# Kernel optimization log

Measured on AMD Instinct MI355X. Metric: run time of the kernel, lower is better.

## Reference

```python
import jax, jax.numpy as jnp
import numpy as np

# Config (matches init_kwargs)
LOW_T = 100      # low_res_timesteps
HIGH_T = 2000    # high_res_timesteps
FEAT = 6         # feature_dim
HID = 256        # student_hidden_dim
NUM_CLASSES = 10
LBL_DIM = 16
UP = HIGH_T // LOW_T  # upsampling_factor = 20
B = 4096


def setup_inputs() -> dict:
    key = jax.random.key(0)
    ks = jax.random.split(key, 20)

    def lin(k, fan_in, fan_out):
        # torch nn.Linear default init: U(-1/sqrt(fan_in), 1/sqrt(fan_in))
        kw, kb = jax.random.split(k)
        bound = 1.0 / np.sqrt(fan_in)
        W = jax.random.uniform(kw, (fan_in, fan_out), jnp.float32, -bound, bound)
        b = jax.random.uniform(kb, (fan_out,), jnp.float32, -bound, bound)
        return W, b

    W1, b1 = lin(ks[0], LOW_T * FEAT, HID * 2)
    W2, b2 = lin(ks[1], HID * 2, HID)
    W3, b3 = lin(ks[2], HID, HID // 2)
    dec_in = HID // 2 + LBL_DIM
    W4, b4 = lin(ks[3], dec_in, HID)
    W5, b5 = lin(ks[4], HID, HID * 2)
    W6, b6 = lin(ks[5], HID * 2, HIGH_T * FEAT)
    emb = jax.random.normal(ks[6], (NUM_CLASSES, LBL_DIM), jnp.float32)

    low_res_data = jax.random.normal(ks[7], (B, LOW_T, FEAT), jnp.float32)
    labels = jax.random.randint(ks[8], (B,), 0, NUM_CLASSES, jnp.int64)
    return {
        'low_res_data': low_res_data, 'labels': labels,
        'W1': W1, 'b1': b1, 'W2': W2, 'b2': b2, 'W3': W3, 'b3': b3,
        'W4': W4, 'b4': b4, 'W5': W5, 'b5': b5, 'W6': W6, 'b6': b6,
        'emb': emb,
    }


def reference(low_res_data, labels, W1, b1, W2, b2, W3, b3, W4, b4, W5, b5, W6, b6, emb):
    batch = low_res_data.shape[0]
    # Encoder MLP (dropout is identity in eval mode)
    x = low_res_data.reshape(batch, -1)                     # [B, LOW_T*FEAT]
    h = jax.nn.relu(x @ W1 + b1)
    h = jax.nn.relu(h @ W2 + b2)
    feat = h @ W3 + b3                                      # [B, HID//2]
    # Label conditioning
    feat = jnp.concatenate([feat, emb[labels]], axis=-1)    # [B, HID//2 + LBL_DIM]
    # Decoder MLP
    h = jax.nn.relu(feat @ W4 + b4)
    h = jax.nn.relu(h @ W5 + b5)
    decoded = (h @ W6 + b6).reshape(batch, HIGH_T, FEAT)    # [B, H, F]

    # Vectorized constraint enforcement + smoothing (replaces per-timestep python loop):
    #  - at anchor timesteps t = i*UP: output = low_res_data[:, i]
    #  - between anchors i and i+1: lin = (1-a)*low[i] + a*low[i+1];
    #      out = lin + 0.2 * (decoded - lin)
    #  - after the last anchor interval ((LOW_T-1)*UP < t < HIGH_T): out = decoded
    t = jnp.arange(HIGH_T)
    seg = jnp.clip(t // UP, 0, LOW_T - 2)                   # segment index per timestep
    alpha = ((t - seg * UP) / UP).astype(decoded.dtype)     # [H], 0 at anchors, 1 at seg end
    start = low_res_data[:, seg]                            # [B, H, F]
    end = low_res_data[:, seg + 1]                          # [B, H, F]
    a = alpha[None, :, None]
    lin_interp = (1.0 - a) * start + a * end                # equals low point at anchors
    blend = lin_interp + 0.2 * (decoded - lin_interp)
    is_anchor = (t % UP == 0)[None, :, None]
    in_interior = (t < (LOW_T - 1) * UP)[None, :, None]
    enhanced = jnp.where(is_anchor, lin_interp, jnp.where(in_interior, blend, decoded))
    return enhanced
```

## Files before the change

### kernel.cpp

```cpp
#include <hip/hip_runtime.h>
#include <hip/hip_bf16.h>

typedef __attribute__((ext_vector_type(8))) short bf16x8;
typedef __attribute__((ext_vector_type(4))) float f32x4;
typedef __attribute__((ext_vector_type(8))) unsigned short u16x8;
typedef unsigned short ushort_t;
typedef unsigned int u32;

__device__ __forceinline__ ushort_t f2b(float f) {
    u32 u = __builtin_bit_cast(u32, f);
    u += 0x7FFFu + ((u >> 16) & 1u);
    return (ushort_t)(u >> 16);
}

__device__ __forceinline__ void gload_lds16(const void* g, void* l) {
    __builtin_amdgcn_global_load_lds(
        (const __attribute__((address_space(1))) u32*)g,
        (__attribute__((address_space(3))) u32*)l, 16, 0, 0);
}

struct TrDesc { const float* src; ushort_t* dst; int K, N, Kpad, Npad, base, nx; };
struct TrArgs { TrDesc d[6]; const float* low; ushort_t* xb; int trbase; };

__global__ __launch_bounds__(256) void prep_kernel(TrArgs a) {
    const int bid = blockIdx.x, tid = threadIdx.x;
    if (bid >= a.trbase) {
        int idx = (bid - a.trbase) * 256 + tid;
        int b = idx / 76, c = idx - b * 76;
        ushort_t* dp = a.xb + (size_t)b * 608 + c * 8;
        u16x8 o;
        if (c < 75) {
            const float* sp = a.low + (size_t)b * 600 + c * 8;
            f32x4 v0 = *(const f32x4*)sp, v1 = *(const f32x4*)(sp + 4);
            #pragma unroll
            for (int j = 0; j < 4; ++j) { o[j] = f2b(v0[j]); o[4 + j] = f2b(v1[j]); }
        } else {
            #pragma unroll
            for (int j = 0; j < 8; ++j) o[j] = 0;
        }
        *(u16x8*)dp = o;
        return;
    }
    __shared__ float T[64][65];
    int w = 0;
    #pragma unroll
    for (int i = 1; i < 6; ++i) if (bid >= a.d[i].base) w = i;
    const TrDesc d = a.d[w];
    const int local = bid - d.base;
    const int n0 = (local % d.nx) * 64, k0 = (local / d.nx) * 64;
    #pragma unroll
    for (int it = 0; it < 16; ++it) {
        int idx = it * 256 + tid;
        int r = idx >> 6, c = idx & 63;
        int k = k0 + r, n = n0 + c;
        T[c][r] = (k < d.K && n < d.N) ? d.src[(size_t)k * d.N + n] : 0.f;
    }
    __syncthreads();
    #pragma unroll
    for (int it = 0; it < 16; ++it) {
        int idx = it * 256 + tid;
        int r = idx >> 6, c = idx & 63;
        int n = n0 + r, k = k0 + c;
        if (k < d.Kpad)
            d.dst[(size_t)n * d.Kpad + k] = f2b(T[r][c]);
    }
}

template<int EPI>
__global__ __launch_bounds__(256, 4) void gemm64(
    const ushort_t* __restrict__ A, const ushort_t* __restrict__ Bt,
    const float* __restrict__ bias, ushort_t* __restrict__ Cb,
    const int* __restrict__ lbl, const float* __restrict__ emb,
    int K, int Nreal, int ldc)
{
    __shared__ ushort_t As[2][64 * 32];
    __shared__ ushort_t Bs[2][64 * 32];
    const int tid = threadIdx.x;
    const int wave = tid >> 6, lane = tid & 63;
    const int l15 = lane & 15, g = lane >> 4;
    const int wr = wave >> 1, wc = wave & 1;
    const int m0 = blockIdx.y * 64, n0 = blockIdx.x * 64;

    f32x4 acc[2][2] = {};

    const int p0 = tid * 16;
    const int row0 = p0 >> 6;
    const int k0s = (((p0 & 63) ^ (((row0 >> 1) & 3) << 4)) >> 1);
    const ushort_t* a0 = A + (size_t)(m0 + row0) * K + k0s;
    const ushort_t* b0 = Bt + (size_t)(n0 + row0) * K + k0s;

    char* AsB = (char*)As + wave * 1024;
    char* BsB = (char*)Bs + wave * 1024;

    const int sxor = ((l15 >> 1) & 3) << 4;
    const ushort_t* ardA = &As[0][0] + (((wr * 32 + l15) * 64 + ((g * 16) ^ sxor)) >> 1);
    const ushort_t* brdB = &Bs[0][0] + (((wc * 32 + l15) * 64 + ((g * 16) ^ sxor)) >> 1);

    const int nk = K >> 5;
    gload_lds16(a0, AsB); gload_lds16(b0, BsB);
    a0 += 32; b0 += 32;
    __syncthreads();
    #pragma unroll 2
    for (int kk = 0; kk < nk; ++kk) {
        const int cur = kk & 1, nxt = cur ^ 1;
        if (kk + 1 < nk) {
            gload_lds16(a0, AsB + nxt * 4096);
            gload_lds16(b0, BsB + nxt * 4096);
            a0 += 32; b0 += 32;
        }
        bf16x8 af[2], bf[2];
        #pragma unroll
        for (int i = 0; i < 2; ++i) af[i] = *(const bf16x8*)(ardA + cur * 2048 + i * 512);
        #pragma unroll
        for (int j = 0; j < 2; ++j) bf[j] = *(const bf16x8*)(brdB + cur * 2048 + j * 512);
        #pragma unroll
        for (int i = 0; i < 2; ++i)
            #pragma unroll
            for (int j = 0; j < 2; ++j)
                acc[i][j] = __builtin_amdgcn_mfma_f32_16x16x32_bf16(af[i], bf[j], acc[i][j], 0, 0, 0);
        __syncthreads();
    }

    #pragma unroll
    for (int i = 0; i < 2; ++i)
        #pragma unroll
        for (int r = 0; r < 4; ++r) {
            int row = m0 + wr * 32 + i * 16 + g * 4 + r;
            #pragma unroll
            for (int j = 0; j < 2; ++j) {
                int col = n0 + wc * 32 + j * 16 + l15;
                if (col >= Nreal) continue;
                float v = acc[i][j][r] + bias[col];
                if (EPI == 0) v = fmaxf(v, 0.f);
                Cb[(size_t)row * ldc + col] = f2b(v);
            }
        }

    if (EPI == 1 && blockIdx.x == 0) {
        #pragma unroll
        for (int q = 0; q < 8; ++q) {
            int e = tid + q * 256;
            int row = m0 + (e >> 5), c = e & 31;
            float v = c < 16 ? emb[(size_t)lbl[row] * 16 + c] : 0.f;
            Cb[(size_t)row * ldc + 128 + c] = f2b(v);
        }
    }
}

__global__ __launch_bounds__(256, 4) void gemm128_l6(
    const ushort_t* __restrict__ A, const ushort_t* __restrict__ Bt,
    const float* __restrict__ bias, float* __restrict__ Cf,
    const float* __restrict__ low, int K)
{
    __shared__ ushort_t As[2][128 * 32];
    __shared__ ushort_t Bs[2][128 * 32];
    const int tid = threadIdx.x;
    const int wave = tid >> 6, lane = tid & 63;
    const int l15 = lane & 15, g = lane >> 4;
    const int wr = wave >> 1, wc = wave & 1;
    const int m0 = blockIdx.y * 128, n0 = blockIdx.x * 128;

    f32x4 acc[4][4] = {};

    const int p0 = tid * 16;
    const int row0 = p0 >> 6;
    const int k0s = (((p0 & 63) ^ (((row0 >> 1) & 3) << 4)) >> 1);
    const int p1 = 4096 + tid * 16;
    const int row1 = p1 >> 6;
    const int k1s = (((p1 & 63) ^ (((row1 >> 1) & 3) << 4)) >> 1);

    const ushort_t* a0 = A + (size_t)(m0 + row0) * K + k0s;
    const ushort_t* a1 = A + (size_t)(m0 + row1) * K + k1s;
    const ushort_t* b0 = Bt + (size_t)(n0 + row0) * K + k0s;
    const ushort_t* b1 = Bt + (size_t)(n0 + row1) * K + k1s;

    char* AsB = (char*)As + wave * 1024;
    char* BsB = (char*)Bs + wave * 1024;

    const int sxor = ((l15 >> 1) & 3) << 4;
    const ushort_t* ardA = &As[0][0] + (((wr * 64 + l15) * 64 + ((g * 16) ^ sxor)) >> 1);
    const ushort_t* brdB = &Bs[0][0] + (((wc * 64 + l15) * 64 + ((g * 16) ^ sxor)) >> 1);

    const int nk = K >> 5;
    gload_lds16(a0, AsB); gload_lds16(a1, AsB + 4096);
    gload_lds16(b0, BsB); gload_lds16(b1, BsB + 4096);
    a0 += 32; a1 += 32; b0 += 32; b1 += 32;
    __syncthreads();
    #pragma unroll 2
    for (int kk = 0; kk < nk; ++kk) {
        const int cur = kk & 1, nxt = cur ^ 1;
        if (kk + 1 < nk) {
            gload_lds16(a0, AsB + nxt * 8192);
            gload_lds16(a1, AsB + nxt * 8192 + 4096);
            gload_lds16(b0, BsB + nxt * 8192);
            gload_lds16(b1, BsB + nxt * 8192 + 4096);
            a0 += 32; a1 += 32; b0 += 32; b1 += 32;
        }
        bf16x8 af[4], bf[4];
        #pragma unroll
        for (int i = 0; i < 4; ++i) af[i] = *(const bf16x8*)(ardA + cur * 4096 + i * 512);
        #pragma unroll
        for (int j = 0; j < 4; ++j) bf[j] = *(const bf16x8*)(brdB + cur * 4096 + j * 512);
        #pragma unroll
        for (int i = 0; i < 4; ++i)
            #pragma unroll
            for (int j = 0; j < 4; ++j)
                acc[i][j] = __builtin_amdgcn_mfma_f32_16x16x32_bf16(af[i], bf[j], acc[i][j], 0, 0, 0);
        __syncthreads();
    }

    float bvv[4]; int offv[4]; float alphav[4];
    bool anch[4], interi[4], valid[4];
    #pragma unroll
    for (int j = 0; j < 4; ++j) {
        int col = n0 + wc * 64 + j * 16 + l15;
        valid[j] = col < 12000;
        int cc = valid[j] ? col : 0;
        bvv[j] = bias[cc];
        int t = cc / 6, f = cc - t * 6;
        int seg = t / 20; if (seg > 98) seg = 98;
        offv[j] = seg * 6 + f;
        alphav[j] = (float)(t - seg * 20) * 0.05f;
        anch[j] = (t % 20) == 0;
        interi[j] = t < 1980;
    }
    const int colb = n0 + wc * 64 + l15;
    #pragma unroll
    for (int i = 0; i < 4; ++i)
        #pragma unroll
        for (int r = 0; r < 4; ++r) {
            const int row = m0 + wr * 64 + i * 16 + g * 4 + r;
            const float* lrow = low + (size_t)row * 600;
            float* orow = Cf + (size_t)row * 12000;
            #pragma unroll
            for (int j = 0; j < 4; ++j) {
                if (!valid[j]) continue;
                float s = lrow[offv[j]], e = lrow[offv[j] + 6];
                float lin = (1.f - alphav[j]) * s + alphav[j] * e;
                float dec = acc[i][j][r] + bvv[j];
                float res = anch[j] ? lin : (interi[j] ? lin + 0.2f * (dec - lin) : dec);
                __builtin_nontemporal_store(res, &orow[colb + j * 16]);
            }
        }
}

extern "C" void kernel_launch(void* const* d_in, const int* in_sizes, int n_in,
                              void* d_out, int out_size, void* d_ws, size_t ws_size,
                              hipStream_t stream) {
    const float* low = (const float*)d_in[0];
    const int*   lbl = (const int*)d_in[1];
    const float* W1 = (const float*)d_in[2];  const float* b1 = (const float*)d_in[3];
    const float* W2 = (const float*)d_in[4];  const float* b2 = (const float*)d_in[5];
    const float* W3 = (const float*)d_in[6];  const float* b3 = (const float*)d_in[7];
    const float* W4 = (const float*)d_in[8];  const float* b4 = (const float*)d_in[9];
    const float* W5 = (const float*)d_in[10]; const float* b5 = (const float*)d_in[11];
    const float* W6 = (const float*)d_in[12]; const float* b6 = (const float*)d_in[13];
    const float* emb = (const float*)d_in[14];
    float* out = (float*)d_out;

    char* ws = (char*)d_ws;
    size_t off = 0;
    auto alloc = [&](size_t elems) {
        ushort_t* p = (ushort_t*)(ws + off);
        off = (off + elems * 2 + 255) & ~(size_t)255;
        return p;
    };
    ushort_t* xb  = alloc((size_t)4096 * 608);
    ushort_t* w1t = alloc((size_t)512 * 608);
    ushort_t* w2t = alloc((size_t)256 * 512);
    ushort_t* w3t = alloc((size_t)128 * 256);
    ushort_t* w4t = alloc((size_t)256 * 160);
    ushort_t* w5t = alloc((size_t)512 * 256);
    ushort_t* w6t = alloc((size_t)12032 * 512);
    ushort_t* h1  = alloc((size_t)4096 * 512);
    ushort_t* h2  = alloc((size_t)4096 * 256);
    ushort_t* fc  = alloc((size_t)4096 * 160);
    ushort_t* h4  = alloc((size_t)4096 * 256);
    ushort_t* h5  = alloc((size_t)4096 * 512);

    TrArgs ta;
    int base = 0;
    auto mk = [&](int i, const float* s, ushort_t* d, int K, int N, int Kp, int Np) {
        int nx = Np / 64, ny = (Kp + 63) / 64;
        ta.d[i] = TrDesc{s, d, K, N, Kp, Np, base, nx};
        base += nx * ny;
    };
    mk(0, W1, w1t, 600, 512, 608, 512);
    mk(1, W2, w2t, 512, 256, 512, 256);
    mk(2, W3, w3t, 256, 128, 256, 128);
    mk(3, W4, w4t, 144, 256, 160, 256);
    mk(4, W5, w5t, 256, 512, 256, 512);
    mk(5, W6, w6t, 512, 12000, 512, 12032);
    ta.low = low; ta.xb = xb; ta.trbase = base;
    const int castx_blocks = (4096 * 76) / 256;

    prep_kernel<<<dim3(base + castx_blocks), 256, 0, stream>>>(ta);

    gemm64<0><<<dim3(8, 64), 256, 0, stream>>>(xb, w1t, b1, h1, nullptr, nullptr, 608, 512, 512);
    gemm64<0><<<dim3(4, 64), 256, 0, stream>>>(h1, w2t, b2, h2, nullptr, nullptr, 512, 256, 256);
    gemm64<1><<<dim3(2, 64), 256, 0, stream>>>(h2, w3t, b3, fc, lbl, emb, 256, 128, 160);
    gemm64<0><<<dim3(4, 64), 256, 0, stream>>>(fc, w4t, b4, h4, nullptr, nullptr, 160, 256, 256);
    gemm64<0><<<dim3(8, 64), 256, 0, stream>>>(h4, w5t, b5, h5, nullptr, nullptr, 256, 512, 512);
    gemm128_l6<<<dim3(94, 32), 256, 0, stream>>>(h5, w6t, b6, out, low, 512);
}
```

Baseline: 392.0 us.

## Fuse prep and first five GEMMs into cooperative kernel; enlarge final GEMM tile

Replaces the prep kernel and five small GEMM launches with one cooperative persistent kernel that uses grid.sync between layers, cutting launch gaps and tail effects. The final layer GEMM moves from 128x128 tiles with 256 threads to 256x256 tiles with 512 threads, which raises data reuse per block but cuts the grid to 752 blocks and adds register pressure. Nontemporal output stores become plain stores. Grid syncs carry their own cost, and the cooperative launch with 512 blocks must fit co-resident on the device.

Result: slower. 983.8 us (+151.0%).

```diff
diff --git a/kernel.cpp b/kernel.cpp
--- a/kernel.cpp
+++ b/kernel.cpp
@@ -1,5 +1,8 @@
 #include <hip/hip_runtime.h>
 #include <hip/hip_bf16.h>
+#include <hip/hip_cooperative_groups.h>
+
+namespace cg = cooperative_groups;
 
 typedef __attribute__((ext_vector_type(8))) short bf16x8;
 typedef __attribute__((ext_vector_type(4))) float f32x4;
@@ -20,66 +23,27 @@
 }
 
 struct TrDesc { const float* src; ushort_t* dst; int K, N, Kpad, Npad, base, nx; };
-struct TrArgs { TrDesc d[6]; const float* low; ushort_t* xb; int trbase; };
-
-__global__ __launch_bounds__(256) void prep_kernel(TrArgs a) {
-    const int bid = blockIdx.x, tid = threadIdx.x;
-    if (bid >= a.trbase) {
-        int idx = (bid - a.trbase) * 256 + tid;
-        int b = idx / 76, c = idx - b * 76;
-        ushort_t* dp = a.xb + (size_t)b * 608 + c * 8;
-        u16x8 o;
-        if (c < 75) {
-            const float* sp = a.low + (size_t)b * 600 + c * 8;
-            f32x4 v0 = *(const f32x4*)sp, v1 = *(const f32x4*)(sp + 4);
-            #pragma unroll
-            for (int j = 0; j < 4; ++j) { o[j] = f2b(v0[j]); o[4 + j] = f2b(v1[j]); }
-        } else {
-            #pragma unroll
-            for (int j = 0; j < 8; ++j) o[j] = 0;
-        }
-        *(u16x8*)dp = o;
-        return;
-    }
-    __shared__ float T[64][65];
-    int w = 0;
-    #pragma unroll
-    for (int i = 1; i < 6; ++i) if (bid >= a.d[i].base) w = i;
-    const TrDesc d = a.d[w];
-    const int local = bid - d.base;
-    const int n0 = (local % d.nx) * 64, k0 = (local / d.nx) * 64;
-    #pragma unroll
-    for (int it = 0; it < 16; ++it) {
-        int idx = it * 256 + tid;
-        int r = idx >> 6, c = idx & 63;
-        int k = k0 + r, n = n0 + c;
-        T[c][r] = (k < d.K && n < d.N) ? d.src[(size_t)k * d.N + n] : 0.f;
-    }
-    __syncthreads();
-    #pragma unroll
-    for (int it = 0; it < 16; ++it) {
-        int idx = it * 256 + tid;
-        int r = idx >> 6, c = idx & 63;
-        int n = n0 + r, k = k0 + c;
-        if (k < d.Kpad)
-            d.dst[(size_t)n * d.Kpad + k] = f2b(T[r][c]);
-    }
-}
-
-template<int EPI>
-__global__ __launch_bounds__(256, 4) void gemm64(
+
+struct CoopArgs {
+    TrDesc d[6];
+    const float* low; const int* lbl; const float* emb;
+    const float *b1, *b2, *b3, *b4, *b5;
+    ushort_t *xb, *h1, *h2, *fc, *h4, *h5;
+    ushort_t *w1t, *w2t, *w3t, *w4t, *w5t;
+    int trbase, total0;
+};
+
+template<int RELU>
+__device__ __forceinline__ void tile_gemm64(
     const ushort_t* __restrict__ A, const ushort_t* __restrict__ Bt,
     const float* __restrict__ bias, ushort_t* __restrict__ Cb,
-    const int* __restrict__ lbl, const float* __restrict__ emb,
-    int K, int Nreal, int ldc)
+    int K, int Nreal, int ldc, int m0, int n0, char* smem, int tid)
 {
-    __shared__ ushort_t As[2][64 * 32];
-    __shared__ ushort_t Bs[2][64 * 32];
-    const int tid = threadIdx.x;
+    ushort_t* As = (ushort_t*)smem;
+    ushort_t* Bs = (ushort_t*)(smem + 8192);
     const int wave = tid >> 6, lane = tid & 63;
     const int l15 = lane & 15, g = lane >> 4;
     const int wr = wave >> 1, wc = wave & 1;
-    const int m0 = blockIdx.y * 64, n0 = blockIdx.x * 64;
 
     f32x4 acc[2][2] = {};
 
@@ -89,18 +53,17 @@
     const ushort_t* a0 = A + (size_t)(m0 + row0) * K + k0s;
     const ushort_t* b0 = Bt + (size_t)(n0 + row0) * K + k0s;
 
-    char* AsB = (char*)As + wave * 1024;
-    char* BsB = (char*)Bs + wave * 1024;
+    char* AsB = smem + wave * 1024;
+    char* BsB = smem + 8192 + wave * 1024;
 
     const int sxor = ((l15 >> 1) & 3) << 4;
-    const ushort_t* ardA = &As[0][0] + (((wr * 32 + l15) * 64 + ((g * 16) ^ sxor)) >> 1);
-    const ushort_t* brdB = &Bs[0][0] + (((wc * 32 + l15) * 64 + ((g * 16) ^ sxor)) >> 1);
+    const ushort_t* ardA = As + (((wr * 32 + l15) * 64 + ((g * 16) ^ sxor)) >> 1);
+    const ushort_t* brdB = Bs + (((wc * 32 + l15) * 64 + ((g * 16) ^ sxor)) >> 1);
 
     const int nk = K >> 5;
     gload_lds16(a0, AsB); gload_lds16(b0, BsB);
     a0 += 32; b0 += 32;
     __syncthreads();
-    #pragma unroll 2
     for (int kk = 0; kk < nk; ++kk) {
         const int cur = kk & 1, nxt = cur ^ 1;
         if (kk + 1 < nk) {
@@ -131,41 +94,115 @@
                 int col = n0 + wc * 32 + j * 16 + l15;
                 if (col >= Nreal) continue;
                 float v = acc[i][j][r] + bias[col];
-                if (EPI == 0) v = fmaxf(v, 0.f);
+                if (RELU) v = fmaxf(v, 0.f);
                 Cb[(size_t)row * ldc + col] = f2b(v);
             }
         }
-
-    if (EPI == 1 && blockIdx.x == 0) {
-        #pragma unroll
-        for (int q = 0; q < 8; ++q) {
-            int e = tid + q * 256;
-            int row = m0 + (e >> 5), c = e & 31;
-            float v = c < 16 ? emb[(size_t)lbl[row] * 16 + c] : 0.f;
-            Cb[(size_t)row * ldc + 128 + c] = f2b(v);
-        }
-    }
-}
-
-__global__ __launch_bounds__(256, 4) void gemm128_l6(
+}
+
+__global__ __launch_bounds__(256) void coop_chain(CoopArgs a) {
+    __shared__ __align__(16) char smem[16640];
+    const int tid = threadIdx.x;
+    const int bid = blockIdx.x;
+    const int nb = gridDim.x;
+    cg::grid_group grid = cg::this_grid();
+
+    for (int u = bid; u < a.total0; u += nb) {
+        if (u < a.trbase) {
+            float (*T)[65] = (float(*)[65])smem;
+            int w = 0;
+            #pragma unroll
+            for (int i = 1; i < 6; ++i) if (u >= a.d[i].base) w = i;
+            const TrDesc d = a.d[w];
+            const int local = u - d.base;
+            const int n0 = (local % d.nx) * 64, k0 = (local / d.nx) * 64;
+            #pragma unroll
+            for (int it = 0; it < 16; ++it) {
+                int idx = it * 256 + tid;
+                int r = idx >> 6, c = idx & 63;
+                int k = k0 + r, n = n0 + c;
+                T[c][r] = (k < d.K && n < d.N) ? d.src[(size_t)k * d.N + n] : 0.f;
+            }
+            __syncthreads();
+            #pragma unroll
+            for (int it = 0; it < 16; ++it) {
+                int idx = it * 256 + tid;
+                int r = idx >> 6, c = idx & 63;
+                int n = n0 + r, k = k0 + c;
+                if (k < d.Kpad)
+                    d.dst[(size_t)n * d.Kpad + k] = f2b(T[r][c]);
+            }
+            __syncthreads();
+        } else {
+            int idx = (u - a.trbase) * 256 + tid;
+            int b = idx / 76, c = idx - b * 76;
+            ushort_t* dp = a.xb + (size_t)b * 608 + c * 8;
+            u16x8 o;
+            if (c < 75) {
+                const float* sp = a.low + (size_t)b * 600 + c * 8;
+                f32x4 v0 = *(const f32x4*)sp, v1 = *(const f32x4*)(sp + 4);
+                #pragma unroll
+                for (int j = 0; j < 4; ++j) { o[j] = f2b(v0[j]); o[4 + j] = f2b(v1[j]); }
+            } else {
+                #pragma unroll
+                for (int j = 0; j < 8; ++j) o[j] = 0;
+            }
+            *(u16x8*)dp = o;
+            __syncthreads();
+        }
+    }
+    __threadfence();
+    grid.sync();
+
+    for (int t = bid; t < 512; t += nb)
+        tile_gemm64<1>(a.xb, a.w1t, a.b1, a.h1, 608, 512, 512, (t >> 3) * 64, (t & 7) * 64, smem, tid);
+    __threadfence();
+    grid.sync();
+
+    for (int t = bid; t < 256; t += nb)
+        tile_gemm64<1>(a.h1, a.w2t, a.b2, a.h2, 512, 256, 256, (t >> 2) * 64, (t & 3) * 64, smem, tid);
+    __threadfence();
+    grid.sync();
+
+    for (int t = bid; t < 128; t += nb)
+        tile_gemm64<0>(a.h2, a.w3t, a.b3, a.fc, 256, 128, 160, (t >> 1) * 64, (t & 1) * 64, smem, tid);
+    for (int u = bid; u < 512; u += nb) {
+        int e = u * 256 + tid;
+        int row = e >> 5, c = e & 31;
+        float v = c < 16 ? a.emb[(size_t)a.lbl[row] * 16 + c] : 0.f;
+        a.fc[(size_t)row * 160 + 128 + c] = f2b(v);
+    }
+    __threadfence();
+    grid.sync();
+
+    for (int t = bid; t < 256; t += nb)
+        tile_gemm64<1>(a.fc, a.w4t, a.b4, a.h4, 160, 256, 256, (t >> 2) * 64, (t & 3) * 64, smem, tid);
+    __threadfence();
+    grid.sync();
+
+    for (int t = bid; t < 512; t += nb)
+        tile_gemm64<1>(a.h4, a.w5t, a.b5, a.h5, 256, 512, 512, (t >> 3) * 64, (t & 7) * 64, smem, tid);
+}
+
+__global__ __launch_bounds__(512) void gemm256_l6(
     const ushort_t* __restrict__ A, const ushort_t* __restrict__ Bt,
     const float* __restrict__ bias, float* __restrict__ Cf,
     const float* __restrict__ low, int K)
 {
-    __shared__ ushort_t As[2][128 * 32];
-    __shared__ ushort_t Bs[2][128 * 32];
+    __shared__ ushort_t As[2][256 * 32];
+    __shared__ ushort_t Bs[2][256 * 32];
     const int tid = threadIdx.x;
     const int wave = tid >> 6, lane = tid & 63;
     const int l15 = lane & 15, g = lane >> 4;
-    const int wr = wave >> 1, wc = wave & 1;
-    const int m0 = blockIdx.y * 128, n0 = blockIdx.x * 128;
-
-    f32x4 acc[4][4] = {};
+    const int wr = wave >> 2, wc = wave & 3;
+    const int m0 = blockIdx.y * 256, n0 = blockIdx.x * 256;
+
+    f32x4 acc[8][4] = {};
 
     const int p0 = tid * 16;
     const int row0 = p0 >> 6;
     const int k0s = (((p0 & 63) ^ (((row0 >> 1) & 3) << 4)) >> 1);
-    const int p1 = 4096 + tid * 16;
+    const int p1 = 8192 + tid * 16;
     const int row1 = p1 >> 6;
     const int k1s = (((p1 & 63) ^ (((row1 >> 1) & 3) << 4)) >> 1);
 
@@ -178,34 +215,33 @@
     char* BsB = (char*)Bs + wave * 1024;
 
     const int sxor = ((l15 >> 1) & 3) << 4;
-    const ushort_t* ardA = &As[0][0] + (((wr * 64 + l15) * 64 + ((g * 16) ^ sxor)) >> 1);
+    const ushort_t* ardA = &As[0][0] + (((wr * 128 + l15) * 64 + ((g * 16) ^ sxor)) >> 1);
     const ushort_t* brdB = &Bs[0][0] + (((wc * 64 + l15) * 64 + ((g * 16) ^ sxor)) >> 1);
 
     const int nk = K >> 5;
-    gload_lds16(a0, AsB); gload_lds16(a1, AsB + 4096);
-    gload_lds16(b0, BsB); gload_lds16(b1, BsB + 4096);
+    gload_lds16(a0, AsB); gload_lds16(a1, AsB + 8192);
+    gload_lds16(b0, BsB); gload_lds16(b1, BsB + 8192);
     a0 += 32; a1 += 32; b0 += 32; b1 += 32;
     __syncthreads();
-    #pragma unroll 2
     for (int kk = 0; kk < nk; ++kk) {
         const int cur = kk & 1, nxt = cur ^ 1;
         if (kk + 1 < nk) {
-            gload_lds16(a0, AsB + nxt * 8192);
-            gload_lds16(a1, AsB + nxt * 8192 + 4096);
-            gload_lds16(b0, BsB + nxt * 8192);
-            gload_lds16(b1, BsB + nxt * 8192 + 4096);
+            gload_lds16(a0, AsB + nxt * 16384);
+            gload_lds16(a1, AsB + nxt * 16384 + 8192);
+            gload_lds16(b0, BsB + nxt * 16384);
+            gload_lds16(b1, BsB + nxt * 16384 + 8192);
             a0 += 32; a1 += 32; b0 += 32; b1 += 32;
         }
-        bf16x8 af[4], bf[4];
-        #pragma unroll
-        for (int i = 0; i < 4; ++i) af[i] = *(const bf16x8*)(ardA + cur * 4096 + i * 512);
-        #pragma unroll
-        for (int j = 0; j < 4; ++j) bf[j] = *(const bf16x8*)(brdB + cur * 4096 + j * 512);
-        #pragma unroll
-        for (int i = 0; i < 4; ++i)
+        bf16x8 bf[4];
+        #pragma unroll
+        for (int j = 0; j < 4; ++j) bf[j] = *(const bf16x8*)(brdB + cur * 8192 + j * 512);
+        #pragma unroll
+        for (int i = 0; i < 8; ++i) {
+            bf16x8 af = *(const bf16x8*)(ardA + cur * 8192 + i * 512);
             #pragma unroll
             for (int j = 0; j < 4; ++j)
-                acc[i][j] = __builtin_amdgcn_mfma_f32_16x16x32_bf16(af[i], bf[j], acc[i][j], 0, 0, 0);
+                acc[i][j] = __builtin_amdgcn_mfma_f32_16x16x32_bf16(af, bf[j], acc[i][j], 0, 0, 0);
+        }
         __syncthreads();
     }
 
@@ -226,10 +262,10 @@
     }
     const int colb = n0 + wc * 64 + l15;
     #pragma unroll
-    for (int i = 0; i < 4; ++i)
+    for (int i = 0; i < 8; ++i)
         #pragma unroll
         for (int r = 0; r < 4; ++r) {
-            const int row = m0 + wr * 64 + i * 16 + g * 4 + r;
+            const int row = m0 + wr * 128 + i * 16 + g * 4 + r;
             const float* lrow = low + (size_t)row * 600;
             float* orow = Cf + (size_t)row * 12000;
             #pragma unroll
@@ -239,7 +275,7 @@
                 float lin = (1.f - alphav[j]) * s + alphav[j] * e;
                 float dec = acc[i][j][r] + bvv[j];
                 float res = anch[j] ? lin : (interi[j] ? lin + 0.2f * (dec - lin) : dec);
-                __builtin_nontemporal_store(res, &orow[colb + j * 16]);
+                orow[colb + j * 16] = res;
             }
         }
 }
@@ -278,11 +314,11 @@
     ushort_t* h4  = alloc((size_t)4096 * 256);
     ushort_t* h5  = alloc((size_t)4096 * 512);
 
-    TrArgs ta;
+    CoopArgs ca;
     int base = 0;
     auto mk = [&](int i, const float* s, ushort_t* d, int K, int N, int Kp, int Np) {
         int nx = Np / 64, ny = (Kp + 63) / 64;
-        ta.d[i] = TrDesc{s, d, K, N, Kp, Np, base, nx};
+        ca.d[i] = TrDesc{s, d, K, N, Kp, Np, base, nx};
         base += nx * ny;
     };
     mk(0, W1, w1t, 600, 512, 608, 512);
@@ -291,15 +327,15 @@
     mk(3, W4, w4t, 144, 256, 160, 256);
     mk(4, W5, w5t, 256, 512, 256, 512);
     mk(5, W6, w6t, 512, 12000, 512, 12032);
-    ta.low = low; ta.xb = xb; ta.trbase = base;
-    const int castx_blocks = (4096 * 76) / 256;
-
-    prep_kernel<<<dim3(base + castx_blocks), 256, 0, stream>>>(ta);
-
-    gemm64<0><<<dim3(8, 64), 256, 0, stream>>>(xb, w1t, b1, h1, nullptr, nullptr, 608, 512, 512);
-    gemm64<0><<<dim3(4, 64), 256, 0, stream>>>(h1, w2t, b2, h2, nullptr, nullptr, 512, 256, 256);
-    gemm64<1><<<dim3(2, 64), 256, 0, stream>>>(h2, w3t, b3, fc, lbl, emb, 256, 128, 160);
-    gemm64<0><<<dim3(4, 64), 256, 0, stream>>>(fc, w4t, b4, h4, nullptr, nullptr, 160, 256, 256);
-    gemm64<0><<<dim3(8, 64), 256, 0, stream>>>(h4, w5t, b5, h5, nullptr, nullptr, 256, 512, 512);
-    gemm128_l6<<<dim3(94, 32), 256, 0, stream>>>(h5, w6t, b6, out, low, 512);
-}
+    ca.low = low; ca.lbl = lbl; ca.emb = emb;
+    ca.b1 = b1; ca.b2 = b2; ca.b3 = b3; ca.b4 = b4; ca.b5 = b5;
+    ca.xb = xb; ca.h1 = h1; ca.h2 = h2; ca.fc = fc; ca.h4 = h4; ca.h5 = h5;
+    ca.w1t = w1t; ca.w2t = w2t; ca.w3t = w3t; ca.w4t = w4t; ca.w5t = w5t;
+    ca.trbase = base;
+    ca.total0 = base + (4096 * 76) / 256;
+
+    void* kp[] = { (void*)&ca };
+    hipLaunchCooperativeKernel((void*)coop_chain, dim3(512), dim3(256), kp, 0, stream);
+
+    gemm256_l6<<<dim3(47, 16), 512, 0, stream>>>(h5, w6t, b6, out, low, 512);
+}
```
